# Kernel optimization log

Hardware: AMD Instinct MI355X
Metric: run time of the kernel (lower is better)

The kernel has to match this reference:

```python
import jax, jax.numpy as jnp
import numpy as np

B, N, C_IN, C_COORD, K = 2, 8192, 64, 3, 16
C_CAT = C_IN + C_COORD  # 67
HID1, HID2, C_OUT = 32, 64, 64


def setup_inputs() -> dict:
    key = jax.random.key(0)
    ks = jax.random.split(key, 10)
    s = 0.05
    return {
        "point_features": jax.random.normal(ks[0], (B, N, C_IN), jnp.float32),
        "coords": jax.random.uniform(ks[1], (B, N, C_COORD), jnp.float32),
        "w1": jax.random.normal(ks[2], (HID1, C_CAT), jnp.float32) * s,
        "b1": jax.random.normal(ks[3], (HID1,), jnp.float32) * s,
        "w2": jax.random.normal(ks[4], (HID2, HID1), jnp.float32) * s,
        "b2": jax.random.normal(ks[5], (HID2,), jnp.float32) * s,
        "w3": jax.random.normal(ks[6], (C_OUT, HID2), jnp.float32) * s,
        "b3": jax.random.normal(ks[7], (C_OUT,), jnp.float32) * s,
        "aggr_w": jax.random.normal(ks[8], (K,), jnp.float32) * s,
        "aggr_b": jax.random.normal(ks[9], (1,), jnp.float32) * s,
    }


def _knn_idx(coords):
    # squared pairwise distances: [B, N, N]
    sq = jnp.sum(coords * coords, axis=-1)
    d2 = sq[:, :, None] + sq[:, None, :] - 2.0 * jnp.einsum("bnc,bmc->bnm", coords, coords)
    # k smallest distances -> top_k of negated; self (d=0) lands at slot 0
    _, idx = jax.lax.top_k(-d2, K)  # [B, N, K]
    return idx


def reference(point_features, coords, w1, b1, w2, b2, w3, b3, aggr_w, aggr_b):
    idx = _knn_idx(coords)  # [B, N, K] int32
    feats = jnp.concatenate([point_features, coords], axis=-1)  # [B, N, C_CAT]
    # gather neighbor features -> [B, N, K, C_CAT]
    g = jax.vmap(lambda f, i: f[i])(feats, idx)
    # relative coords w.r.t. neighbor 0 (self)
    rel = g[..., -C_COORD:] - g[:, :, 0:1, -C_COORD:]
    g = jnp.concatenate([g[..., :C_IN], rel], axis=-1)
    # point pooling: max over K of raw input-feature channels
    y_pool = jnp.max(g[..., :C_IN], axis=2)  # [B, N, C_IN]
    # kernel MLP: stacked 1x1 convs, NO activations (act_func=None in source)
    h = jnp.einsum("bnkc,oc->bnko", g, w1) + b1
    h = jnp.einsum("bnkc,oc->bnko", h, w2) + b2
    h = jnp.einsum("bnkc,oc->bnko", h, w3) + b3  # [B, N, K, C_OUT]
    # attentive aggregation: Conv2d(K, 1, 1) over the K axis
    y_aggr = jnp.einsum("bnko,k->bno", h, aggr_w) + aggr_b  # [B, N, C_OUT]
    out_sum = jnp.sum(h, axis=2)  # [B, N, C_OUT]
    # concat order matches torch: (sum, pool, aggr), then permute -> B x N x C'
    return jnp.concatenate([out_sum, y_pool, y_aggr], axis=-1)
```

## Files before the change

### kernel.cpp

```cpp
#include <hip/hip_runtime.h>
#include <stdint.h>


typedef unsigned short u16;
typedef unsigned int   u32;
typedef unsigned long long u64;

#define NPTS  8192
#define KNB   16
#define SCAP  128
#define QPW   8

__device__ __forceinline__ float bf2f(u16 u) {
    union { u32 i; float f; } v; v.i = ((u32)u) << 16; return v.f;
}
__device__ __forceinline__ u16 f2bf(float f) {
    u32 x = __float_as_uint(f);
    return (u16)((x + 0x7FFFu + ((x >> 16) & 1u)) >> 16);
}
__device__ __forceinline__ u32 fordkey(float f) {
    u32 u = __float_as_uint(f);
    return u ^ ((u32)((int)u >> 31) | 0x80000000u);
}
__device__ __forceinline__ u64 shflxor64(u64 v, int m) {
    int lo = __shfl_xor((int)(u32)v, m, 64);
    int hi = __shfl_xor((int)(u32)(v >> 32), m, 64);
    return ((u64)(u32)hi << 32) | (u32)lo;
}
__device__ __forceinline__ float sq_np32(float x, float y, float z) {
    return __fadd_rn(__fadd_rn(__fmul_rn(x, x), __fmul_rn(y, y)), __fmul_rn(z, z));
}
__device__ __forceinline__ float d2_ref(float qx, float qy, float qz, float qsq,
                                        float x, float y, float z, float sq) {
    float dot = fmaf(z, qz, fmaf(y, qy, __fmul_rn(x, qx)));
    return __fsub_rn(__fadd_rn(qsq, sq), __fmul_rn(2.0f, dot));
}
__device__ __forceinline__ int cellof(float v) {
    int c = (int)floorf(v * 8.0f);
    return c < 0 ? 0 : (c > 7 ? 7 : c);
}

__global__ __launch_bounds__(256) void pack_count_kernel(
    const float* __restrict__ pf, const float* __restrict__ coords,
    u16* __restrict__ pfh, int* __restrict__ counts) {
    int gid = blockIdx.x * 256 + threadIdx.x;
    pfh[gid] = f2bf(pf[gid]);
    if (gid < 2 * NPTS) {
        float x = coords[gid * 3 + 0];
        float y = coords[gid * 3 + 1];
        float z = coords[gid * 3 + 2];
        int b = gid >> 13;
        int cell = (cellof(x) * 8 + cellof(y)) * 8 + cellof(z);
        atomicAdd(&counts[b * 512 + cell], 1);
    }
}

__global__ __launch_bounds__(512) void scan_kernel(
    const int* __restrict__ counts, int* __restrict__ cellStart,
    int* __restrict__ cellOffset) {
    __shared__ int s[512];
    int b = blockIdx.x, t = threadIdx.x;
    int myc = counts[b * 512 + t];
    s[t] = myc; __syncthreads();
#pragma unroll
    for (int off = 1; off < 512; off <<= 1) {
        int v = (t >= off) ? s[t - off] : 0; __syncthreads();
        s[t] += v; __syncthreads();
    }
    int excl = s[t] - myc;
    cellStart[b * 513 + t] = excl;
    cellOffset[b * 512 + t] = excl;
    if (t == 511) cellStart[b * 513 + 512] = s[511];
}

__global__ __launch_bounds__(256) void scatter_kernel(
    const float* __restrict__ coords, int* __restrict__ cellOffset,
    float4* __restrict__ spts, int* __restrict__ sidx) {
    int gid = blockIdx.x * 256 + threadIdx.x;
    float x = coords[gid * 3 + 0];
    float y = coords[gid * 3 + 1];
    float z = coords[gid * 3 + 2];
    int b = gid >> 13, i = gid & (NPTS - 1);
    int cell = (cellof(x) * 8 + cellof(y)) * 8 + cellof(z);
    int pos = atomicAdd(&cellOffset[b * 512 + cell], 1);
    spts[b * NPTS + pos] = make_float4(x, y, z, sq_np32(x, y, z));
    sidx[b * NPTS + pos] = i;
}

__global__ __launch_bounds__(64, 4) void knn_kernel(
    const float* __restrict__ coords, const float4* __restrict__ spts,
    const int* __restrict__ sidx, const int* __restrict__ cellStart,
    int* __restrict__ idx_out) {
    __shared__ u64 surv[SCAP];

    const int lane = threadIdx.x;
    const int blk  = blockIdx.x;
    const int b    = blk >> 11;
    const int q0   = (blk & 2047) * 4;
    const float*  cb = coords + (size_t)b * NPTS * 3;
    const float4* sp = spts + b * NPTS;
    const int*    si = sidx + b * NPTS;
    const int*    cs = cellStart + b * 513;

#pragma unroll 1
    for (int t = 0; t < 4; ++t) {
        const int q = q0 + t;
        float qx = cb[q * 3 + 0], qy = cb[q * 3 + 1], qz = cb[q * 3 + 2];
        float qsq = sq_np32(qx, qy, qz);
        int cqx = cellof(qx), cqy = cellof(qy), cqz = cellof(qz);

        int ax0 = max(cqx - 1, 0), ax1 = min(cqx + 1, 7);
        int ay0 = max(cqy - 1, 0), ay1 = min(cqy + 1, 7);
        int az0 = max(cqz - 1, 0), az1 = min(cqz + 1, 7);
        float dmin = 3.0e38f;
#pragma unroll 1
        for (int cx = ax0; cx <= ax1; ++cx)
#pragma unroll 1
            for (int cy = ay0; cy <= ay1; ++cy) {
                int base = (cx * 8 + cy) * 8;
                int s = cs[base + az0], e = cs[base + az1 + 1];
                for (int i0 = s; i0 < e; i0 += 64) {
                    int i = i0 + lane;
                    int ii = (i < e) ? i : (e - 1);
                    float4 c = sp[ii];
                    float d2 = d2_ref(qx, qy, qz, qsq, c.x, c.y, c.z, c.w);
                    if (i < e) dmin = fminf(dmin, d2);
                }
            }
        {
            float v = dmin;
#pragma unroll
            for (int k = 2; k <= 64; k <<= 1) {
#pragma unroll
                for (int j2 = k >> 1; j2 >= 1; j2 >>= 1) {
                    float o = __shfl_xor(v, j2, 64);
                    bool lo = (lane & j2) == 0;
                    bool up = (lane & k) == 0;
                    float mn = fminf(v, o), mx = fmaxf(v, o);
                    v = (lo == up) ? mn : mx;
                }
            }
            dmin = __shfl(v, 15, 64);
        }
        const float tau = dmin;

        float rr = sqrtf(tau + 1e-5f) + 1e-6f;
        int bx0 = max((int)floorf((qx - rr) * 8.0f), 0);
        int bx1 = min((int)floorf((qx + rr) * 8.0f), 7);
        int by0 = max((int)floorf((qy - rr) * 8.0f), 0);
        int by1 = min((int)floorf((qy + rr) * 8.0f), 7);
        int bz0 = max((int)floorf((qz - rr) * 8.0f), 0);
        int bz1 = min((int)floorf((qz + rr) * 8.0f), 7);
        int cnt = 0;
#pragma unroll 1
        for (int cx = bx0; cx <= bx1; ++cx)
#pragma unroll 1
            for (int cy = by0; cy <= by1; ++cy) {
                int base = (cx * 8 + cy) * 8;
                int s = cs[base + bz0], e = cs[base + bz1 + 1];
                for (int i0 = s; i0 < e; i0 += 64) {
                    int i = i0 + lane;
                    bool valid = (i < e);
                    int ii = valid ? i : (e - 1);
                    float4 c = sp[ii];
                    float d2 = d2_ref(qx, qy, qz, qsq, c.x, c.y, c.z, c.w);
                    bool pass = valid && (d2 <= tau);
                    u64 mask = __ballot(pass);
                    if (pass) {
                        int pre = __builtin_amdgcn_mbcnt_hi((u32)(mask >> 32),
                                  __builtin_amdgcn_mbcnt_lo((u32)mask, 0));
                        int pos = cnt + pre;
                        if (pos < SCAP)
                            surv[pos] = ((u64)fordkey(d2) << 32) | (u32)si[ii];
                    }
                    cnt += (int)__popcll(mask);
                }
            }
        __syncthreads();

        int myidx = 0;
        if (cnt <= 64) {
            u64 key = (lane < cnt) ? surv[lane] : ~0ull;
#pragma unroll
            for (int k = 2; k <= 64; k <<= 1) {
#pragma unroll
                for (int j2 = k >> 1; j2 >= 1; j2 >>= 1) {
                    u64 o = shflxor64(key, j2);
                    bool lo = (lane & j2) == 0;
                    bool up = (lane & k) == 0;
                    bool takemin = (lo == up);
                    key = ((o < key) == takemin) ? o : key;
                }
            }
            myidx = (int)(u32)(key & 0xffffffffu);
        } else {
            int cc = cnt > SCAP ? SCAP : cnt;
            u64 a0 = (lane < cc) ? surv[lane] : ~0ull;
            u64 a1 = (64 + lane < cc) ? surv[64 + lane] : ~0ull;
            if (a1 < a0) { u64 tmp = a0; a0 = a1; a1 = tmp; }
#pragma unroll 1
            for (int r = 0; r < 16; ++r) {
                u64 m = a0;
#pragma unroll
                for (int d = 1; d < 64; d <<= 1) {
                    u64 o = shflxor64(m, d);
                    m = (o < m) ? o : m;
                }
                if (a0 == m) { a0 = a1; a1 = ~0ull; }
                if (lane == r) myidx = (int)(u32)(m & 0xffffffffu);
            }
        }
        if (lane < KNB)
            idx_out[((size_t)b * NPTS + q) * KNB + lane] = myidx;
        __syncthreads();
    }
}

__global__ __launch_bounds__(64) void mlp_kernel(
    const u16* __restrict__ pfh, const float* __restrict__ coords,
    const float* __restrict__ w1, const float* __restrict__ b1,
    const float* __restrict__ w2, const float* __restrict__ b2,
    const float* __restrict__ w3, const float* __restrict__ b3,
    const float* __restrict__ aw, const float* __restrict__ ab,
    const int* __restrict__ knn_idx, float* __restrict__ out) {

    __shared__ __attribute__((aligned(16))) float vbuf[2][68];
    __shared__ __attribute__((aligned(16))) float h1buf[2][36];

    const int lane = threadIdx.x;
    const int r    = lane & 31;
    const int vec  = lane >> 5;

    float w1r[68];
#pragma unroll
    for (int c = 0; c < 67; ++c) w1r[c] = w1[r * 67 + c];
    w1r[67] = 0.0f;
    float w2r[32];
    {
        const float4* p = (const float4*)(w2 + lane * 32);
#pragma unroll
        for (int c4 = 0; c4 < 8; ++c4) {
            float4 v = p[c4];
            w2r[c4 * 4 + 0] = v.x; w2r[c4 * 4 + 1] = v.y;
            w2r[c4 * 4 + 2] = v.z; w2r[c4 * 4 + 3] = v.w;
        }
    }
    float w3r[64];
    {
        const float4* p = (const float4*)(w3 + lane * 64);
#pragma unroll
        for (int c4 = 0; c4 < 16; ++c4) {
            float4 v = p[c4];
            w3r[c4 * 4 + 0] = v.x; w3r[c4 * 4 + 1] = v.y;
            w3r[c4 * 4 + 2] = v.z; w3r[c4 * 4 + 3] = v.w;
        }
    }
    float awr[16];
#pragma unroll
    for (int k = 0; k < 16; ++k) awr[k] = aw[k];
    float sa = 0.0f;
#pragma unroll
    for (int k = 0; k < 16; ++k) sa += awr[k];
    const float b1v = b1[r], b2v = b2[lane], b3v = b3[lane], abv = ab[0];
    const float c1 = (vec == 0) ? 16.0f : sa;

#pragma unroll 1
    for (int t = 0; t < QPW; ++t) {
        const int gq = blockIdx.x * QPW + t;
        const int b  = gq >> 13;
        const u16*   pfb = pfh + (size_t)b * NPTS * 64;
        const float* cb  = coords + (size_t)b * NPTS * 3;

        int myi = knn_idx[(size_t)gq * KNB + (lane & 15)] & (NPTS - 1);

        float pool = -3.0e38f, G1 = 0.0f, Ga = 0.0f;
#pragma unroll
        for (int k = 0; k < 16; ++k) {
            int nk = __shfl(myi, k, 64);
            float v = bf2f(pfb[nk * 64 + lane]);
            pool = fmaxf(pool, v);
            G1 += v;
            Ga = fmaf(awr[k], v, Ga);
        }
        vbuf[0][lane] = G1;
        vbuf[1][lane] = Ga;

        if (lane < 48) {
            int j  = lane >> 4;
            int i0 = __shfl(myi, 0, 64);
            float rel  = cb[myi * 3 + j] - cb[i0 * 3 + j];
            float wrel = awr[lane & 15] * rel;
#pragma unroll
            for (int d = 1; d < 16; d <<= 1) {
                rel  += __shfl_xor(rel, d, 64);
                wrel += __shfl_xor(wrel, d, 64);
            }
            if ((lane & 15) == 0) { vbuf[0][64 + j] = rel; vbuf[1][64 + j] = wrel; }
        }
        if (lane == 0) { vbuf[0][67] = 0.0f; vbuf[1][67] = 0.0f; }
        __syncthreads();

        float acc = c1 * b1v;
        {
            const float4* vp = (const float4*)(&vbuf[vec][0]);
#pragma unroll
            for (int c4 = 0; c4 < 17; ++c4) {
                float4 g4 = vp[c4];
                acc = fmaf(g4.x, w1r[c4 * 4 + 0], acc);
                acc = fmaf(g4.y, w1r[c4 * 4 + 1], acc);
                acc = fmaf(g4.z, w1r[c4 * 4 + 2], acc);
                acc = fmaf(g4.w, w1r[c4 * 4 + 3], acc);
            }
        }
        h1buf[vec][r] = acc;
        __syncthreads();

        float a0 = 16.0f * b2v, a1 = sa * b2v;
        {
            const float4* p0 = (const float4*)(&h1buf[0][0]);
            const float4* p1 = (const float4*)(&h1buf[1][0]);
#pragma unroll
            for (int c4 = 0; c4 < 8; ++c4) {
                float4 x0 = p0[c4], x1 = p1[c4];
                a0 = fmaf(x0.x, w2r[c4 * 4 + 0], a0);
                a0 = fmaf(x0.y, w2r[c4 * 4 + 1], a0);
                a0 = fmaf(x0.z, w2r[c4 * 4 + 2], a0);
                a0 = fmaf(x0.w, w2r[c4 * 4 + 3], a0);
                a1 = fmaf(x1.x, w2r[c4 * 4 + 0], a1);
                a1 = fmaf(x1.y, w2r[c4 * 4 + 1], a1);
                a1 = fmaf(x1.z, w2r[c4 * 4 + 2], a1);
                a1 = fmaf(x1.w, w2r[c4 * 4 + 3], a1);
            }
        }
        __syncthreads();
        vbuf[0][lane] = a0;
        vbuf[1][lane] = a1;
        __syncthreads();

        float s1 = 16.0f * b3v, sA = sa * b3v;
        {
            const float4* p0 = (const float4*)(&vbuf[0][0]);
            const float4* p1 = (const float4*)(&vbuf[1][0]);
#pragma unroll
            for (int c4 = 0; c4 < 16; ++c4) {
                float4 x0 = p0[c4], x1 = p1[c4];
                s1 = fmaf(x0.x, w3r[c4 * 4 + 0], s1);
                s1 = fmaf(x0.y, w3r[c4 * 4 + 1], s1);
                s1 = fmaf(x0.z, w3r[c4 * 4 + 2], s1);
                s1 = fmaf(x0.w, w3r[c4 * 4 + 3], s1);
                sA = fmaf(x1.x, w3r[c4 * 4 + 0], sA);
                sA = fmaf(x1.y, w3r[c4 * 4 + 1], sA);
                sA = fmaf(x1.z, w3r[c4 * 4 + 2], sA);
                sA = fmaf(x1.w, w3r[c4 * 4 + 3], sA);
            }
        }
        float* op = out + (size_t)gq * 192;
        op[lane]       = s1;
        op[64 + lane]  = pool;
        op[128 + lane] = sA + abv;
        __syncthreads();
    }
}

extern "C" void kernel_launch(void* const* d_in, const int* in_sizes, int n_in,
                              void* d_out, int out_size, void* d_ws, size_t ws_size,
                              hipStream_t stream) {
    const float* pf     = (const float*)d_in[0];
    const float* coords = (const float*)d_in[1];
    const float* w1     = (const float*)d_in[2];
    const float* b1     = (const float*)d_in[3];
    const float* w2     = (const float*)d_in[4];
    const float* b2     = (const float*)d_in[5];
    const float* w3     = (const float*)d_in[6];
    const float* b3     = (const float*)d_in[7];
    const float* aw     = (const float*)d_in[8];
    const float* ab     = (const float*)d_in[9];

    char* ws = (char*)d_ws;
    int*    knn_idx    = (int*)ws;
    u16*    pfh        = (u16*)(ws + (1 << 20));
    float4* spts       = (float4*)(ws + (3 << 20));
    int*    sidx       = (int*)(ws + (3 << 20) + (256 << 10));
    int*    cellStart  = (int*)(ws + (3 << 20) + (320 << 10));
    int*    counts     = (int*)(ws + (3 << 20) + (328 << 10));
    int*    cellOffset = (int*)(ws + (3 << 20) + (336 << 10));
    float*  outp       = (float*)d_out;

    hipMemsetAsync(counts, 0, 2 * 512 * sizeof(int), stream);
    pack_count_kernel<<<4096, 256, 0, stream>>>(pf, coords, pfh, counts);
    scan_kernel<<<2, 512, 0, stream>>>(counts, cellStart, cellOffset);
    scatter_kernel<<<64, 256, 0, stream>>>(coords, cellOffset, spts, sidx);
    knn_kernel<<<4096, 64, 0, stream>>>(coords, spts, sidx, cellStart, knn_idx);
    mlp_kernel<<<2048, 64, 0, stream>>>(pfh, coords, w1, b1, w2, b2, w3, b3,
                                        aw, ab, knn_idx, outp);
}
```

Measured before the change: 153.6 us.

## Fuse kNN with MLP, merge scan and scatter, process queries in cell order

The kNN search and the MLP now run in one kernel, so neighbour indices stay in registers and are never written to or read back from global memory. The scan and scatter kernels are merged into a single two-block kernel that uses shared-memory atomics for the cell offsets. Queries are taken in spatially sorted order via sidx, and blocks are interleaved across the grid, to improve locality. The risks are higher register pressure from loading the MLP weights after the kNN phase, lower occupancy without the (64,4) launch bound, and a scatter now carried by only two blocks.

```diff
diff --git a/kernel.cpp b/kernel.cpp
--- a/kernel.cpp
+++ b/kernel.cpp
@@ -9,7 +9,6 @@
 #define NPTS  8192
 #define KNB   16
 #define SCAP  128
-#define QPW   8
 
 __device__ __forceinline__ float bf2f(u16 u) {
     union { u32 i; float f; } v; v.i = ((u32)u) << 16; return v.f;
@@ -55,56 +54,69 @@
     }
 }
 
-__global__ __launch_bounds__(512) void scan_kernel(
-    const int* __restrict__ counts, int* __restrict__ cellStart,
-    int* __restrict__ cellOffset) {
+__global__ __launch_bounds__(512) void scan_scatter_kernel(
+    const int* __restrict__ counts, const float* __restrict__ coords,
+    int* __restrict__ cellStart, float4* __restrict__ spts,
+    int* __restrict__ sidx) {
     __shared__ int s[512];
+    __shared__ int off[512];
     int b = blockIdx.x, t = threadIdx.x;
     int myc = counts[b * 512 + t];
     s[t] = myc; __syncthreads();
 #pragma unroll
-    for (int off = 1; off < 512; off <<= 1) {
-        int v = (t >= off) ? s[t - off] : 0; __syncthreads();
+    for (int o = 1; o < 512; o <<= 1) {
+        int v = (t >= o) ? s[t - o] : 0; __syncthreads();
         s[t] += v; __syncthreads();
     }
     int excl = s[t] - myc;
     cellStart[b * 513 + t] = excl;
-    cellOffset[b * 512 + t] = excl;
+    off[t] = excl;
     if (t == 511) cellStart[b * 513 + 512] = s[511];
-}
-
-__global__ __launch_bounds__(256) void scatter_kernel(
-    const float* __restrict__ coords, int* __restrict__ cellOffset,
-    float4* __restrict__ spts, int* __restrict__ sidx) {
-    int gid = blockIdx.x * 256 + threadIdx.x;
-    float x = coords[gid * 3 + 0];
-    float y = coords[gid * 3 + 1];
-    float z = coords[gid * 3 + 2];
-    int b = gid >> 13, i = gid & (NPTS - 1);
-    int cell = (cellof(x) * 8 + cellof(y)) * 8 + cellof(z);
-    int pos = atomicAdd(&cellOffset[b * 512 + cell], 1);
-    spts[b * NPTS + pos] = make_float4(x, y, z, sq_np32(x, y, z));
-    sidx[b * NPTS + pos] = i;
-}
-
-__global__ __launch_bounds__(64, 4) void knn_kernel(
+    __syncthreads();
+
+    const float* cb = coords + (size_t)b * NPTS * 3;
+#pragma unroll 1
+    for (int k = 0; k < 16; ++k) {
+        int i = k * 512 + t;
+        float x = cb[i * 3 + 0];
+        float y = cb[i * 3 + 1];
+        float z = cb[i * 3 + 2];
+        int cell = (cellof(x) * 8 + cellof(y)) * 8 + cellof(z);
+        int pos = atomicAdd(&off[cell], 1);
+        spts[b * NPTS + pos] = make_float4(x, y, z, sq_np32(x, y, z));
+        sidx[b * NPTS + pos] = i;
+    }
+}
+
+__global__ __launch_bounds__(64) void knnmlp_kernel(
     const float* __restrict__ coords, const float4* __restrict__ spts,
     const int* __restrict__ sidx, const int* __restrict__ cellStart,
-    int* __restrict__ idx_out) {
+    const u16* __restrict__ pfh,
+    const float* __restrict__ w1, const float* __restrict__ b1,
+    const float* __restrict__ w2, const float* __restrict__ b2,
+    const float* __restrict__ w3, const float* __restrict__ b3,
+    const float* __restrict__ aw, const float* __restrict__ ab,
+    float* __restrict__ out) {
     __shared__ u64 surv[SCAP];
+    __shared__ __attribute__((aligned(16))) float vbuf[2][68];
+    __shared__ __attribute__((aligned(16))) float h1buf[2][36];
 
     const int lane = threadIdx.x;
-    const int blk  = blockIdx.x;
-    const int b    = blk >> 11;
-    const int q0   = (blk & 2047) * 4;
+    const int sblk = (blockIdx.x & 7) * 512 + (blockIdx.x >> 3);
+    const int b    = sblk >> 11;
+    const int p0   = (sblk & 2047) * 4;
     const float*  cb = coords + (size_t)b * NPTS * 3;
     const float4* sp = spts + b * NPTS;
     const int*    si = sidx + b * NPTS;
     const int*    cs = cellStart + b * 513;
 
+    int qarr[4];
+    int midx[4];
+
 #pragma unroll 1
     for (int t = 0; t < 4; ++t) {
-        const int q = q0 + t;
+        const int q = si[p0 + t];
+        qarr[t] = q;
         float qx = cb[q * 3 + 0], qy = cb[q * 3 + 1], qz = cb[q * 3 + 2];
         float qsq = sq_np32(qx, qy, qz);
         int cqx = cellof(qx), cqy = cellof(qy), cqz = cellof(qz);
@@ -210,27 +222,14 @@
                 if (lane == r) myidx = (int)(u32)(m & 0xffffffffu);
             }
         }
-        if (lane < KNB)
-            idx_out[((size_t)b * NPTS + q) * KNB + lane] = myidx;
-        __syncthreads();
-    }
-}
-
-__global__ __launch_bounds__(64) void mlp_kernel(
-    const u16* __restrict__ pfh, const float* __restrict__ coords,
-    const float* __restrict__ w1, const float* __restrict__ b1,
-    const float* __restrict__ w2, const float* __restrict__ b2,
-    const float* __restrict__ w3, const float* __restrict__ b3,
-    const float* __restrict__ aw, const float* __restrict__ ab,
-    const int* __restrict__ knn_idx, float* __restrict__ out) {
-
-    __shared__ __attribute__((aligned(16))) float vbuf[2][68];
-    __shared__ __attribute__((aligned(16))) float h1buf[2][36];
-
-    const int lane = threadIdx.x;
-    const int r    = lane & 31;
-    const int vec  = lane >> 5;
-
+        midx[t] = myidx;
+        __syncthreads();
+    }
+
+    __builtin_amdgcn_sched_barrier(0);
+
+    const int r   = lane & 31;
+    const int vec = lane >> 5;
     float w1r[68];
 #pragma unroll
     for (int c = 0; c < 67; ++c) w1r[c] = w1[r * 67 + c];
@@ -263,15 +262,12 @@
     for (int k = 0; k < 16; ++k) sa += awr[k];
     const float b1v = b1[r], b2v = b2[lane], b3v = b3[lane], abv = ab[0];
     const float c1 = (vec == 0) ? 16.0f : sa;
-
-#pragma unroll 1
-    for (int t = 0; t < QPW; ++t) {
-        const int gq = blockIdx.x * QPW + t;
-        const int b  = gq >> 13;
-        const u16*   pfb = pfh + (size_t)b * NPTS * 64;
-        const float* cb  = coords + (size_t)b * NPTS * 3;
-
-        int myi = knn_idx[(size_t)gq * KNB + (lane & 15)] & (NPTS - 1);
+    const u16* pfb = pfh + (size_t)b * NPTS * 64;
+
+#pragma unroll 1
+    for (int t = 0; t < 4; ++t) {
+        const int gq = b * NPTS + qarr[t];
+        int myi = __shfl(midx[t], lane & 15, 64);
 
         float pool = -3.0e38f, G1 = 0.0f, Ga = 0.0f;
 #pragma unroll
@@ -377,20 +373,17 @@
     const float* ab     = (const float*)d_in[9];
 
     char* ws = (char*)d_ws;
-    int*    knn_idx    = (int*)ws;
-    u16*    pfh        = (u16*)(ws + (1 << 20));
-    float4* spts       = (float4*)(ws + (3 << 20));
-    int*    sidx       = (int*)(ws + (3 << 20) + (256 << 10));
-    int*    cellStart  = (int*)(ws + (3 << 20) + (320 << 10));
-    int*    counts     = (int*)(ws + (3 << 20) + (328 << 10));
-    int*    cellOffset = (int*)(ws + (3 << 20) + (336 << 10));
+    u16*    pfh        = (u16*)ws;
+    float4* spts       = (float4*)(ws + (2 << 20));
+    int*    sidx       = (int*)(ws + (2 << 20) + (256 << 10));
+    int*    cellStart  = (int*)(ws + (2 << 20) + (320 << 10));
+    int*    counts     = (int*)(ws + (2 << 20) + (328 << 10));
     float*  outp       = (float*)d_out;
 
     hipMemsetAsync(counts, 0, 2 * 512 * sizeof(int), stream);
     pack_count_kernel<<<4096, 256, 0, stream>>>(pf, coords, pfh, counts);
-    scan_kernel<<<2, 512, 0, stream>>>(counts, cellStart, cellOffset);
-    scatter_kernel<<<64, 256, 0, stream>>>(coords, cellOffset, spts, sidx);
-    knn_kernel<<<4096, 64, 0, stream>>>(coords, spts, sidx, cellStart, knn_idx);
-    mlp_kernel<<<2048, 64, 0, stream>>>(pfh, coords, w1, b1, w2, b2, w3, b3,
-                                        aw, ab, knn_idx, outp);
-}
+    scan_scatter_kernel<<<2, 512, 0, stream>>>(counts, coords, cellStart,
+                                               spts, sidx);
+    knnmlp_kernel<<<4096, 64, 0, stream>>>(coords, spts, sidx, cellStart, pfh,
+                                           w1, b1, w2, b2, w3, b3, aw, ab, outp);
+}
```

Result: slower. 183.9 us (+19.7%).

## Collapse linear MLP into one matrix and fuse kNN with aggregation

Applied to the files above, without the earlier changes.

Since the MLP has no activations, a one-block prep kernel precomputes the collapsed 64x67 weight M=W3·W2·W1 and the collapsed bias, so each query needs a single 67-wide matvec instead of three layers. The kNN search and the MLP/aggregation are fused into one kernel with one query per wave, which removes the knn_idx round trip through global memory and one launch. Queries are also processed in cell-sorted order with a block swizzle to improve neighbour locality. Collapsing the layers changes the floating-point rounding order, and the per-wave LDS sync now relies on __threadfence_block rather than a barrier.

```diff
diff --git a/kernel.cpp b/kernel.cpp
--- a/kernel.cpp
+++ b/kernel.cpp
@@ -9,7 +9,6 @@
 #define NPTS  8192
 #define KNB   16
 #define SCAP  128
-#define QPW   8
 
 __device__ __forceinline__ float bf2f(u16 u) {
     union { u32 i; float f; } v; v.i = ((u32)u) << 16; return v.f;
@@ -63,8 +62,8 @@
     int myc = counts[b * 512 + t];
     s[t] = myc; __syncthreads();
 #pragma unroll
-    for (int off = 1; off < 512; off <<= 1) {
-        int v = (t >= off) ? s[t - off] : 0; __syncthreads();
+    for (int o = 1; o < 512; o <<= 1) {
+        int v = (t >= o) ? s[t - o] : 0; __syncthreads();
         s[t] += v; __syncthreads();
     }
     int excl = s[t] - myc;
@@ -87,279 +86,240 @@
     sidx[b * NPTS + pos] = i;
 }
 
-__global__ __launch_bounds__(64, 4) void knn_kernel(
+__global__ __launch_bounds__(64) void prep_kernel(
+    const float* __restrict__ w1, const float* __restrict__ b1,
+    const float* __restrict__ w2, const float* __restrict__ b2,
+    const float* __restrict__ w3, const float* __restrict__ b3,
+    float* __restrict__ M, float* __restrict__ E) {
+    __shared__ float W1s[32 * 67];
+    __shared__ float W2s[64 * 32];
+    __shared__ float W3s[64 * 64];
+    __shared__ float T[64][68];
+    __shared__ float tb2[64];
+    int t = threadIdx.x;
+    for (int i = t; i < 32 * 67; i += 64) W1s[i] = w1[i];
+    for (int i = t; i < 64 * 32; i += 64) W2s[i] = w2[i];
+    for (int i = t; i < 64 * 64; i += 64) W3s[i] = w3[i];
+    __syncthreads();
+    {
+        float accb = 0.0f;
+#pragma unroll
+        for (int i = 0; i < 32; ++i) accb = fmaf(W2s[t * 32 + i], b1[i], accb);
+        tb2[t] = accb + b2[t];
+#pragma unroll 1
+        for (int c = 0; c < 67; ++c) {
+            float acc = 0.0f;
+#pragma unroll
+            for (int i = 0; i < 32; ++i)
+                acc = fmaf(W2s[t * 32 + i], W1s[i * 67 + c], acc);
+            T[t][c] = acc;
+        }
+        T[t][67] = 0.0f;
+    }
+    __syncthreads();
+#pragma unroll 1
+    for (int c = 0; c < 67; ++c) {
+        float acc = 0.0f;
+#pragma unroll
+        for (int j = 0; j < 64; ++j)
+            acc = fmaf(W3s[t * 64 + j], T[j][c], acc);
+        M[t * 68 + c] = acc;
+    }
+    M[t * 68 + 67] = 0.0f;
+    float e = 0.0f;
+#pragma unroll
+    for (int j = 0; j < 64; ++j) e = fmaf(W3s[t * 64 + j], tb2[j], e);
+    E[t] = e + b3[t];
+}
+
+__global__ __launch_bounds__(128) void knnmlp_kernel(
     const float* __restrict__ coords, const float4* __restrict__ spts,
     const int* __restrict__ sidx, const int* __restrict__ cellStart,
-    int* __restrict__ idx_out) {
-    __shared__ u64 surv[SCAP];
-
-    const int lane = threadIdx.x;
-    const int blk  = blockIdx.x;
-    const int b    = blk >> 11;
-    const int q0   = (blk & 2047) * 4;
+    const u16* __restrict__ pfh, const float* __restrict__ M,
+    const float* __restrict__ E, const float* __restrict__ aw,
+    const float* __restrict__ ab, float* __restrict__ out) {
+
+    __shared__ u64 surv[2][SCAP];
+    __shared__ __attribute__((aligned(16))) float vb[2][2][68];
+
+    const int lane = threadIdx.x & 63;
+    const int wv   = threadIdx.x >> 6;
+    const int sblk = ((int)blockIdx.x & 7) * 1024 + ((int)blockIdx.x >> 3);
+    const int pos  = sblk * 2 + wv;
+    const int b    = pos >> 13;
+    const int p    = pos & (NPTS - 1);
     const float*  cb = coords + (size_t)b * NPTS * 3;
     const float4* sp = spts + b * NPTS;
     const int*    si = sidx + b * NPTS;
     const int*    cs = cellStart + b * 513;
-
-#pragma unroll 1
-    for (int t = 0; t < 4; ++t) {
-        const int q = q0 + t;
-        float qx = cb[q * 3 + 0], qy = cb[q * 3 + 1], qz = cb[q * 3 + 2];
-        float qsq = sq_np32(qx, qy, qz);
-        int cqx = cellof(qx), cqy = cellof(qy), cqz = cellof(qz);
-
-        int ax0 = max(cqx - 1, 0), ax1 = min(cqx + 1, 7);
-        int ay0 = max(cqy - 1, 0), ay1 = min(cqy + 1, 7);
-        int az0 = max(cqz - 1, 0), az1 = min(cqz + 1, 7);
-        float dmin = 3.0e38f;
-#pragma unroll 1
-        for (int cx = ax0; cx <= ax1; ++cx)
-#pragma unroll 1
-            for (int cy = ay0; cy <= ay1; ++cy) {
-                int base = (cx * 8 + cy) * 8;
-                int s = cs[base + az0], e = cs[base + az1 + 1];
-                for (int i0 = s; i0 < e; i0 += 64) {
-                    int i = i0 + lane;
-                    int ii = (i < e) ? i : (e - 1);
-                    float4 c = sp[ii];
-                    float d2 = d2_ref(qx, qy, qz, qsq, c.x, c.y, c.z, c.w);
-                    if (i < e) dmin = fminf(dmin, d2);
+    u64* sv = surv[wv];
+
+    const int q = si[p];
+    float qx = cb[q * 3 + 0], qy = cb[q * 3 + 1], qz = cb[q * 3 + 2];
+    float qsq = sq_np32(qx, qy, qz);
+    int cqx = cellof(qx), cqy = cellof(qy), cqz = cellof(qz);
+
+    int ax0 = max(cqx - 1, 0), ax1 = min(cqx + 1, 7);
+    int ay0 = max(cqy - 1, 0), ay1 = min(cqy + 1, 7);
+    int az0 = max(cqz - 1, 0), az1 = min(cqz + 1, 7);
+    float dmin = 3.0e38f;
+#pragma unroll 1
+    for (int cx = ax0; cx <= ax1; ++cx)
+#pragma unroll 1
+        for (int cy = ay0; cy <= ay1; ++cy) {
+            int base = (cx * 8 + cy) * 8;
+            int s = cs[base + az0], e = cs[base + az1 + 1];
+            for (int i0 = s; i0 < e; i0 += 64) {
+                int i = i0 + lane;
+                int ii = (i < e) ? i : (e - 1);
+                float4 c = sp[ii];
+                float d2 = d2_ref(qx, qy, qz, qsq, c.x, c.y, c.z, c.w);
+                if (i < e) dmin = fminf(dmin, d2);
+            }
+        }
+    {
+        float v = dmin;
+#pragma unroll
+        for (int k = 2; k <= 64; k <<= 1) {
+#pragma unroll
+            for (int j2 = k >> 1; j2 >= 1; j2 >>= 1) {
+                float o = __shfl_xor(v, j2, 64);
+                bool lo = (lane & j2) == 0;
+                bool up = (lane & k) == 0;
+                float mn = fminf(v, o), mx = fmaxf(v, o);
+                v = (lo == up) ? mn : mx;
+            }
+        }
+        dmin = __shfl(v, 15, 64);
+    }
+    const float tau = dmin;
+
+    float rr = sqrtf(tau + 1e-5f) + 1e-6f;
+    int bx0 = max((int)floorf((qx - rr) * 8.0f), 0);
+    int bx1 = min((int)floorf((qx + rr) * 8.0f), 7);
+    int by0 = max((int)floorf((qy - rr) * 8.0f), 0);
+    int by1 = min((int)floorf((qy + rr) * 8.0f), 7);
+    int bz0 = max((int)floorf((qz - rr) * 8.0f), 0);
+    int bz1 = min((int)floorf((qz + rr) * 8.0f), 7);
+    int cnt = 0;
+#pragma unroll 1
+    for (int cx = bx0; cx <= bx1; ++cx)
+#pragma unroll 1
+        for (int cy = by0; cy <= by1; ++cy) {
+            int base = (cx * 8 + cy) * 8;
+            int s = cs[base + bz0], e = cs[base + bz1 + 1];
+            for (int i0 = s; i0 < e; i0 += 64) {
+                int i = i0 + lane;
+                bool valid = (i < e);
+                int ii = valid ? i : (e - 1);
+                float4 c = sp[ii];
+                float d2 = d2_ref(qx, qy, qz, qsq, c.x, c.y, c.z, c.w);
+                bool pass = valid && (d2 <= tau);
+                u64 mask = __ballot(pass);
+                if (pass) {
+                    int pre = __builtin_amdgcn_mbcnt_hi((u32)(mask >> 32),
+                              __builtin_amdgcn_mbcnt_lo((u32)mask, 0));
+                    int pp = cnt + pre;
+                    if (pp < SCAP)
+                        sv[pp] = ((u64)fordkey(d2) << 32) | (u32)si[ii];
                 }
-            }
-        {
-            float v = dmin;
-#pragma unroll
-            for (int k = 2; k <= 64; k <<= 1) {
-#pragma unroll
-                for (int j2 = k >> 1; j2 >= 1; j2 >>= 1) {
-                    float o = __shfl_xor(v, j2, 64);
-                    bool lo = (lane & j2) == 0;
-                    bool up = (lane & k) == 0;
-                    float mn = fminf(v, o), mx = fmaxf(v, o);
-                    v = (lo == up) ? mn : mx;
-                }
-            }
-            dmin = __shfl(v, 15, 64);
-        }
-        const float tau = dmin;
-
-        float rr = sqrtf(tau + 1e-5f) + 1e-6f;
-        int bx0 = max((int)floorf((qx - rr) * 8.0f), 0);
-        int bx1 = min((int)floorf((qx + rr) * 8.0f), 7);
-        int by0 = max((int)floorf((qy - rr) * 8.0f), 0);
-        int by1 = min((int)floorf((qy + rr) * 8.0f), 7);
-        int bz0 = max((int)floorf((qz - rr) * 8.0f), 0);
-        int bz1 = min((int)floorf((qz + rr) * 8.0f), 7);
-        int cnt = 0;
-#pragma unroll 1
-        for (int cx = bx0; cx <= bx1; ++cx)
-#pragma unroll 1
-            for (int cy = by0; cy <= by1; ++cy) {
-                int base = (cx * 8 + cy) * 8;
-                int s = cs[base + bz0], e = cs[base + bz1 + 1];
-                for (int i0 = s; i0 < e; i0 += 64) {
-                    int i = i0 + lane;
-                    bool valid = (i < e);
-                    int ii = valid ? i : (e - 1);
-                    float4 c = sp[ii];
-                    float d2 = d2_ref(qx, qy, qz, qsq, c.x, c.y, c.z, c.w);
-                    bool pass = valid && (d2 <= tau);
-                    u64 mask = __ballot(pass);
-                    if (pass) {
-                        int pre = __builtin_amdgcn_mbcnt_hi((u32)(mask >> 32),
-                                  __builtin_amdgcn_mbcnt_lo((u32)mask, 0));
-                        int pos = cnt + pre;
-                        if (pos < SCAP)
-                            surv[pos] = ((u64)fordkey(d2) << 32) | (u32)si[ii];
-                    }
-                    cnt += (int)__popcll(mask);
-                }
-            }
-        __syncthreads();
-
-        int myidx = 0;
-        if (cnt <= 64) {
-            u64 key = (lane < cnt) ? surv[lane] : ~0ull;
-#pragma unroll
-            for (int k = 2; k <= 64; k <<= 1) {
-#pragma unroll
-                for (int j2 = k >> 1; j2 >= 1; j2 >>= 1) {
-                    u64 o = shflxor64(key, j2);
-                    bool lo = (lane & j2) == 0;
-                    bool up = (lane & k) == 0;
-                    bool takemin = (lo == up);
-                    key = ((o < key) == takemin) ? o : key;
-                }
-            }
-            myidx = (int)(u32)(key & 0xffffffffu);
-        } else {
-            int cc = cnt > SCAP ? SCAP : cnt;
-            u64 a0 = (lane < cc) ? surv[lane] : ~0ull;
-            u64 a1 = (64 + lane < cc) ? surv[64 + lane] : ~0ull;
-            if (a1 < a0) { u64 tmp = a0; a0 = a1; a1 = tmp; }
-#pragma unroll 1
-            for (int r = 0; r < 16; ++r) {
-                u64 m = a0;
-#pragma unroll
-                for (int d = 1; d < 64; d <<= 1) {
-                    u64 o = shflxor64(m, d);
-                    m = (o < m) ? o : m;
-                }
-                if (a0 == m) { a0 = a1; a1 = ~0ull; }
-                if (lane == r) myidx = (int)(u32)(m & 0xffffffffu);
-            }
-        }
-        if (lane < KNB)
-            idx_out[((size_t)b * NPTS + q) * KNB + lane] = myidx;
-        __syncthreads();
-    }
-}
-
-__global__ __launch_bounds__(64) void mlp_kernel(
-    const u16* __restrict__ pfh, const float* __restrict__ coords,
-    const float* __restrict__ w1, const float* __restrict__ b1,
-    const float* __restrict__ w2, const float* __restrict__ b2,
-    const float* __restrict__ w3, const float* __restrict__ b3,
-    const float* __restrict__ aw, const float* __restrict__ ab,
-    const int* __restrict__ knn_idx, float* __restrict__ out) {
-
-    __shared__ __attribute__((aligned(16))) float vbuf[2][68];
-    __shared__ __attribute__((aligned(16))) float h1buf[2][36];
-
-    const int lane = threadIdx.x;
-    const int r    = lane & 31;
-    const int vec  = lane >> 5;
-
-    float w1r[68];
-#pragma unroll
-    for (int c = 0; c < 67; ++c) w1r[c] = w1[r * 67 + c];
-    w1r[67] = 0.0f;
-    float w2r[32];
-    {
-        const float4* p = (const float4*)(w2 + lane * 32);
-#pragma unroll
-        for (int c4 = 0; c4 < 8; ++c4) {
-            float4 v = p[c4];
-            w2r[c4 * 4 + 0] = v.x; w2r[c4 * 4 + 1] = v.y;
-            w2r[c4 * 4 + 2] = v.z; w2r[c4 * 4 + 3] = v.w;
-        }
-    }
-    float w3r[64];
-    {
-        const float4* p = (const float4*)(w3 + lane * 64);
-#pragma unroll
-        for (int c4 = 0; c4 < 16; ++c4) {
-            float4 v = p[c4];
-            w3r[c4 * 4 + 0] = v.x; w3r[c4 * 4 + 1] = v.y;
-            w3r[c4 * 4 + 2] = v.z; w3r[c4 * 4 + 3] = v.w;
-        }
-    }
+                cnt += (int)__popcll(mask);
+            }
+        }
+    __threadfence_block();
+
+    int myidx = 0;
+    if (cnt <= 64) {
+        u64 key = (lane < cnt) ? sv[lane] : ~0ull;
+#pragma unroll
+        for (int k = 2; k <= 64; k <<= 1) {
+#pragma unroll
+            for (int j2 = k >> 1; j2 >= 1; j2 >>= 1) {
+                u64 o = shflxor64(key, j2);
+                bool lo = (lane & j2) == 0;
+                bool up = (lane & k) == 0;
+                bool takemin = (lo == up);
+                key = ((o < key) == takemin) ? o : key;
+            }
+        }
+        myidx = (int)(u32)(key & 0xffffffffu);
+    } else {
+        int cc = cnt > SCAP ? SCAP : cnt;
+        u64 a0 = (lane < cc) ? sv[lane] : ~0ull;
+        u64 a1 = (64 + lane < cc) ? sv[64 + lane] : ~0ull;
+        if (a1 < a0) { u64 tmp = a0; a0 = a1; a1 = tmp; }
+#pragma unroll 1
+        for (int r2 = 0; r2 < 16; ++r2) {
+            u64 mm = a0;
+#pragma unroll
+            for (int d = 1; d < 64; d <<= 1) {
+                u64 o = shflxor64(mm, d);
+                mm = (o < mm) ? o : mm;
+            }
+            if (a0 == mm) { a0 = a1; a1 = ~0ull; }
+            if (lane == r2) myidx = (int)(u32)(mm & 0xffffffffu);
+        }
+    }
+
+    __builtin_amdgcn_sched_barrier(0);
+
     float awr[16];
 #pragma unroll
     for (int k = 0; k < 16; ++k) awr[k] = aw[k];
     float sa = 0.0f;
 #pragma unroll
     for (int k = 0; k < 16; ++k) sa += awr[k];
-    const float b1v = b1[r], b2v = b2[lane], b3v = b3[lane], abv = ab[0];
-    const float c1 = (vec == 0) ? 16.0f : sa;
-
-#pragma unroll 1
-    for (int t = 0; t < QPW; ++t) {
-        const int gq = blockIdx.x * QPW + t;
-        const int b  = gq >> 13;
-        const u16*   pfb = pfh + (size_t)b * NPTS * 64;
-        const float* cb  = coords + (size_t)b * NPTS * 3;
-
-        int myi = knn_idx[(size_t)gq * KNB + (lane & 15)] & (NPTS - 1);
-
-        float pool = -3.0e38f, G1 = 0.0f, Ga = 0.0f;
-#pragma unroll
-        for (int k = 0; k < 16; ++k) {
-            int nk = __shfl(myi, k, 64);
-            float v = bf2f(pfb[nk * 64 + lane]);
-            pool = fmaxf(pool, v);
-            G1 += v;
-            Ga = fmaf(awr[k], v, Ga);
-        }
-        vbuf[0][lane] = G1;
-        vbuf[1][lane] = Ga;
-
-        if (lane < 48) {
-            int j  = lane >> 4;
-            int i0 = __shfl(myi, 0, 64);
-            float rel  = cb[myi * 3 + j] - cb[i0 * 3 + j];
-            float wrel = awr[lane & 15] * rel;
-#pragma unroll
-            for (int d = 1; d < 16; d <<= 1) {
-                rel  += __shfl_xor(rel, d, 64);
-                wrel += __shfl_xor(wrel, d, 64);
-            }
-            if ((lane & 15) == 0) { vbuf[0][64 + j] = rel; vbuf[1][64 + j] = wrel; }
-        }
-        if (lane == 0) { vbuf[0][67] = 0.0f; vbuf[1][67] = 0.0f; }
-        __syncthreads();
-
-        float acc = c1 * b1v;
-        {
-            const float4* vp = (const float4*)(&vbuf[vec][0]);
-#pragma unroll
-            for (int c4 = 0; c4 < 17; ++c4) {
-                float4 g4 = vp[c4];
-                acc = fmaf(g4.x, w1r[c4 * 4 + 0], acc);
-                acc = fmaf(g4.y, w1r[c4 * 4 + 1], acc);
-                acc = fmaf(g4.z, w1r[c4 * 4 + 2], acc);
-                acc = fmaf(g4.w, w1r[c4 * 4 + 3], acc);
-            }
-        }
-        h1buf[vec][r] = acc;
-        __syncthreads();
-
-        float a0 = 16.0f * b2v, a1 = sa * b2v;
-        {
-            const float4* p0 = (const float4*)(&h1buf[0][0]);
-            const float4* p1 = (const float4*)(&h1buf[1][0]);
-#pragma unroll
-            for (int c4 = 0; c4 < 8; ++c4) {
-                float4 x0 = p0[c4], x1 = p1[c4];
-                a0 = fmaf(x0.x, w2r[c4 * 4 + 0], a0);
-                a0 = fmaf(x0.y, w2r[c4 * 4 + 1], a0);
-                a0 = fmaf(x0.z, w2r[c4 * 4 + 2], a0);
-                a0 = fmaf(x0.w, w2r[c4 * 4 + 3], a0);
-                a1 = fmaf(x1.x, w2r[c4 * 4 + 0], a1);
-                a1 = fmaf(x1.y, w2r[c4 * 4 + 1], a1);
-                a1 = fmaf(x1.z, w2r[c4 * 4 + 2], a1);
-                a1 = fmaf(x1.w, w2r[c4 * 4 + 3], a1);
-            }
-        }
-        __syncthreads();
-        vbuf[0][lane] = a0;
-        vbuf[1][lane] = a1;
-        __syncthreads();
-
-        float s1 = 16.0f * b3v, sA = sa * b3v;
-        {
-            const float4* p0 = (const float4*)(&vbuf[0][0]);
-            const float4* p1 = (const float4*)(&vbuf[1][0]);
-#pragma unroll
-            for (int c4 = 0; c4 < 16; ++c4) {
-                float4 x0 = p0[c4], x1 = p1[c4];
-                s1 = fmaf(x0.x, w3r[c4 * 4 + 0], s1);
-                s1 = fmaf(x0.y, w3r[c4 * 4 + 1], s1);
-                s1 = fmaf(x0.z, w3r[c4 * 4 + 2], s1);
-                s1 = fmaf(x0.w, w3r[c4 * 4 + 3], s1);
-                sA = fmaf(x1.x, w3r[c4 * 4 + 0], sA);
-                sA = fmaf(x1.y, w3r[c4 * 4 + 1], sA);
-                sA = fmaf(x1.z, w3r[c4 * 4 + 2], sA);
-                sA = fmaf(x1.w, w3r[c4 * 4 + 3], sA);
-            }
-        }
-        float* op = out + (size_t)gq * 192;
-        op[lane]       = s1;
-        op[64 + lane]  = pool;
-        op[128 + lane] = sA + abv;
-        __syncthreads();
-    }
+    const float ev = E[lane], abv = ab[0];
+    const u16* pfb = pfh + (size_t)b * NPTS * 64;
+
+    float pool = -3.0e38f, G1 = 0.0f, Ga = 0.0f;
+#pragma unroll
+    for (int k = 0; k < 16; ++k) {
+        int nk = __shfl(myidx, k, 64);
+        float v = bf2f(pfb[nk * 64 + lane]);
+        pool = fmaxf(pool, v);
+        G1 += v;
+        Ga = fmaf(awr[k], v, Ga);
+    }
+    float* v0 = vb[wv][0];
+    float* v1 = vb[wv][1];
+    v0[lane] = G1;
+    v1[lane] = Ga;
+    if (lane < 48) {
+        int j1 = lane >> 4;
+        int nk2 = __shfl(myidx, lane & 15, 64);
+        int i0  = __shfl(myidx, 0, 64);
+        float rel  = cb[nk2 * 3 + j1] - cb[i0 * 3 + j1];
+        float wrel = awr[lane & 15] * rel;
+#pragma unroll
+        for (int d = 1; d < 16; d <<= 1) {
+            rel  += __shfl_xor(rel, d, 64);
+            wrel += __shfl_xor(wrel, d, 64);
+        }
+        if ((lane & 15) == 0) { v0[64 + j1] = rel; v1[64 + j1] = wrel; }
+    }
+    if (lane == 0) { v0[67] = 0.0f; v1[67] = 0.0f; }
+    __threadfence_block();
+
+    float s1 = 16.0f * ev, sA = sa * ev;
+    {
+        const float4* mp = (const float4*)(M + lane * 68);
+        const float4* p0 = (const float4*)v0;
+        const float4* p1 = (const float4*)v1;
+#pragma unroll
+        for (int c4 = 0; c4 < 17; ++c4) {
+            float4 mr = mp[c4];
+            float4 x0 = p0[c4], x1 = p1[c4];
+            s1 = fmaf(x0.x, mr.x, s1); s1 = fmaf(x0.y, mr.y, s1);
+            s1 = fmaf(x0.z, mr.z, s1); s1 = fmaf(x0.w, mr.w, s1);
+            sA = fmaf(x1.x, mr.x, sA); sA = fmaf(x1.y, mr.y, sA);
+            sA = fmaf(x1.z, mr.z, sA); sA = fmaf(x1.w, mr.w, sA);
+        }
+    }
+    float* op = out + ((size_t)b * NPTS + q) * 192;
+    op[lane]       = s1;
+    op[64 + lane]  = pool;
+    op[128 + lane] = sA + abv;
 }
 
 extern "C" void kernel_launch(void* const* d_in, const int* in_sizes, int n_in,
@@ -377,20 +337,21 @@
     const float* ab     = (const float*)d_in[9];
 
     char* ws = (char*)d_ws;
-    int*    knn_idx    = (int*)ws;
-    u16*    pfh        = (u16*)(ws + (1 << 20));
-    float4* spts       = (float4*)(ws + (3 << 20));
-    int*    sidx       = (int*)(ws + (3 << 20) + (256 << 10));
-    int*    cellStart  = (int*)(ws + (3 << 20) + (320 << 10));
-    int*    counts     = (int*)(ws + (3 << 20) + (328 << 10));
-    int*    cellOffset = (int*)(ws + (3 << 20) + (336 << 10));
+    u16*    pfh        = (u16*)ws;
+    float4* spts       = (float4*)(ws + (2 << 20));
+    int*    sidx       = (int*)(ws + (2 << 20) + (256 << 10));
+    int*    cellStart  = (int*)(ws + (2 << 20) + (320 << 10));
+    int*    counts     = (int*)(ws + (2 << 20) + (328 << 10));
+    int*    cellOffset = (int*)(ws + (2 << 20) + (336 << 10));
+    float*  Mw         = (float*)(ws + (2 << 20) + (344 << 10));
+    float*  Ew         = (float*)(ws + (2 << 20) + (364 << 10));
     float*  outp       = (float*)d_out;
 
     hipMemsetAsync(counts, 0, 2 * 512 * sizeof(int), stream);
     pack_count_kernel<<<4096, 256, 0, stream>>>(pf, coords, pfh, counts);
     scan_kernel<<<2, 512, 0, stream>>>(counts, cellStart, cellOffset);
     scatter_kernel<<<64, 256, 0, stream>>>(coords, cellOffset, spts, sidx);
-    knn_kernel<<<4096, 64, 0, stream>>>(coords, spts, sidx, cellStart, knn_idx);
-    mlp_kernel<<<2048, 64, 0, stream>>>(pfh, coords, w1, b1, w2, b2, w3, b3,
-                                        aw, ab, knn_idx, outp);
-}
+    prep_kernel<<<1, 64, 0, stream>>>(w1, b1, w2, b2, w3, b3, Mw, Ew);
+    knnmlp_kernel<<<8192, 128, 0, stream>>>(coords, spts, sidx, cellStart, pfh,
+                                            Mw, Ew, aw, ab, outp);
+}
```

Result: slower. 181.2 us (+18.0%).
